# Performance work log

Measured on AMD Instinct MI355X. Metric: run time of the kernel, lower is better.

Reference implementation:

```python
import jax, jax.numpy as jnp
import numpy as np

E = 128       # embedding_size
H = 4         # num_heads
D = E // H    # head_dim = 32
PAD = 16      # window_size; full window width = 2*PAD+1 = 33
B = 4
N = 8192


def setup_inputs() -> dict:
    key = jax.random.key(0)
    ks = jax.random.split(key, 9)
    s = 1.0 / np.sqrt(E)
    return {
        "q": jax.random.normal(ks[0], (B, N, E), dtype=jnp.float32),
        "Wq_w": jax.random.normal(ks[1], (E, E), dtype=jnp.float32) * s,
        "Wq_b": jax.random.normal(ks[2], (E,), dtype=jnp.float32) * s,
        "Wk_w": jax.random.normal(ks[3], (E, E), dtype=jnp.float32) * s,
        "Wk_b": jax.random.normal(ks[4], (E,), dtype=jnp.float32) * s,
        "Wv_w": jax.random.normal(ks[5], (E, E), dtype=jnp.float32) * s,
        "Wv_b": jax.random.normal(ks[6], (E,), dtype=jnp.float32) * s,
        "Wo_w": jax.random.normal(ks[7], (E, E), dtype=jnp.float32) * s,
        "Wo_b": jax.random.normal(ks[8], (E,), dtype=jnp.float32) * s,
    }


def reference(q, Wq_w, Wq_b, Wk_w, Wk_b, Wv_w, Wv_b, Wo_w, Wo_b):
    # Self-attention: k = v = q (forward defaults).
    Q = q @ Wq_w.T + Wq_b
    K = q @ Wk_w.T + Wk_b
    V = q @ Wv_w.T + Wv_b
    b, n, _ = Q.shape
    # (b, H, n, D)
    Q = Q.reshape(b, n, H, D).transpose(0, 2, 1, 3)
    K = K.reshape(b, n, H, D).transpose(0, 2, 1, 3)
    V = V.reshape(b, n, H, D).transpose(0, 2, 1, 3)
    W = 2 * PAD + 1
    # Zero-pad the sequence dim (matches F.pad: padded keys are zero vectors,
    # included in softmax WITHOUT masking — faithful to the original).
    K_pad = jnp.pad(K, ((0, 0), (0, 0), (PAD, PAD), (0, 0)))
    V_pad = jnp.pad(V, ((0, 0), (0, 0), (PAD, PAD), (0, 0)))
    # Window gather indices: row n sees padded positions n .. n+2*PAD
    idx = jnp.arange(n)[:, None] + jnp.arange(W)[None, :]  # (n, W)
    K_win = K_pad[:, :, idx]  # (b, H, n, W, D)
    V_win = V_pad[:, :, idx]  # (b, H, n, W, D)
    scores = jnp.einsum("bhnd,bhnwd->bhnw", Q, K_win) / jnp.sqrt(
        jnp.asarray(D, dtype=Q.dtype)
    )
    probs = jax.nn.softmax(scores, axis=-1)  # dropout is identity in eval
    out = jnp.einsum("bhnw,bhnwd->bhnd", probs, V_win)
    out = out.transpose(0, 2, 1, 3).reshape(b, n, E)
    out = out @ Wo_w.T + Wo_b
    return out, probs
```

## Files before the change

### kernel.cpp

```cpp
#include <hip/hip_runtime.h>

#define BN 4
#define NN 8192
#define EE 128
#define HH 4
#define DD 32
#define WW 33
#define MROWS (BN*NN)
#define QELEMS (MROWS*EE)
#define WELEMS (EE*EE)
#define RT 8

typedef __bf16 bf16x8 __attribute__((ext_vector_type(8)));
typedef float f32x4 __attribute__((ext_vector_type(4)));
typedef unsigned short u16x8 __attribute__((ext_vector_type(8)));

static __device__ __forceinline__ unsigned short f2bf(float x){
    unsigned u = __float_as_uint(x);
    u += 0x7fffu + ((u >> 16) & 1u);
    return (unsigned short)(u >> 16);
}
static __device__ __forceinline__ float bf2f(unsigned short h){
    return __uint_as_float(((unsigned)h) << 16);
}
static __device__ __forceinline__ bf16x8 ld_bf8(const unsigned short* p){
    u16x8 v = *(const u16x8*)p;
    return __builtin_bit_cast(bf16x8, v);
}

__global__ void __launch_bounds__(256) prep_w(const float* __restrict__ wq, const float* __restrict__ wk,
        const float* __restrict__ wv, const float* __restrict__ wo,
        unsigned short* __restrict__ wh, unsigned short* __restrict__ wl){
    int i = blockIdx.x*256 + threadIdx.x;
    int sel = i >> 14;
    const float* src = (sel==0)? wq : (sel==1)? wk : (sel==2)? wv : wo;
    float x = src[i & (WELEMS-1)];
    unsigned short h = f2bf(x);
    wh[i] = h;
    wl[i] = f2bf(x - bf2f(h));
}

__global__ void __launch_bounds__(512,2) gemm_qkv(const float* __restrict__ q,
        const unsigned short* __restrict__ wh, const unsigned short* __restrict__ wl,
        const float* __restrict__ bq, const float* __restrict__ bk, const float* __restrict__ bv_,
        float* __restrict__ Qf, float* __restrict__ Kf, float* __restrict__ Vf)
{
    const int w = threadIdx.x >> 6;
    const int lane = threadIdx.x & 63;
    const int m = lane & 15, g = lane >> 4;
    const int rowB = blockIdx.x * (16*RT);

    bf16x8 bH[3][4], bL[3][4];
    #pragma unroll
    for (int i=0;i<3;i++){
        const unsigned short* WHp = wh + i*WELEMS + (size_t)(w*16 + m)*EE;
        const unsigned short* WLp = wl + i*WELEMS + (size_t)(w*16 + m)*EE;
        #pragma unroll
        for (int kc=0;kc<4;kc++){
            bH[i][kc] = ld_bf8(WHp + kc*32 + g*8);
            bL[i][kc] = ld_bf8(WLp + kc*32 + g*8);
        }
    }
    const float bias[3] = { bq[w*16+m], bk[w*16+m], bv_[w*16+m] };
    float* const outp[3] = { Qf, Kf, Vf };

    float4 fa[2][8];
    {
        const float* qrow = q + (size_t)(rowB + m) * EE;
        #pragma unroll
        for (int kc=0;kc<4;kc++){
            fa[0][kc*2]   = *(const float4*)(qrow + kc*32 + g*8);
            fa[0][kc*2+1] = *(const float4*)(qrow + kc*32 + g*8 + 4);
        }
    }
    #pragma unroll
    for (int rt=0; rt<RT; rt++){
        const int row0 = rowB + rt*16;
        if (rt+1 < RT){
            const float* qrow = q + (size_t)(row0 + 16 + m) * EE;
            #pragma unroll
            for (int kc=0;kc<4;kc++){
                fa[(rt+1)&1][kc*2]   = *(const float4*)(qrow + kc*32 + g*8);
                fa[(rt+1)&1][kc*2+1] = *(const float4*)(qrow + kc*32 + g*8 + 4);
            }
        }
        bf16x8 aH[4], aL[4];
        #pragma unroll
        for (int kc=0;kc<4;kc++){
            float4 v0 = fa[rt&1][kc*2], v1 = fa[rt&1][kc*2+1];
            float vv[8] = {v0.x,v0.y,v0.z,v0.w,v1.x,v1.y,v1.z,v1.w};
            u16x8 hh, ll;
            #pragma unroll
            for (int j=0;j<8;j++){
                unsigned short h = f2bf(vv[j]);
                hh[j] = h;
                ll[j] = f2bf(vv[j] - bf2f(h));
            }
            aH[kc] = __builtin_bit_cast(bf16x8, hh);
            aL[kc] = __builtin_bit_cast(bf16x8, ll);
        }
        #pragma unroll
        for (int i=0;i<3;i++){
            f32x4 acc = {0.f,0.f,0.f,0.f};
            #pragma unroll
            for (int kc=0;kc<4;kc++){
                acc = __builtin_amdgcn_mfma_f32_16x16x32_bf16(aH[kc], bH[i][kc], acc, 0,0,0);
                acc = __builtin_amdgcn_mfma_f32_16x16x32_bf16(aH[kc], bL[i][kc], acc, 0,0,0);
                acc = __builtin_amdgcn_mfma_f32_16x16x32_bf16(aL[kc], bH[i][kc], acc, 0,0,0);
            }
            float* op = outp[i] + (size_t)(row0 + g*4)*EE + w*16 + m;
            #pragma unroll
            for (int r=0;r<4;r++) op[(size_t)r*EE] = acc[r] + bias[i];
        }
    }
}

__global__ void __launch_bounds__(512,2) gemm_o(const unsigned short* __restrict__ ah,
        const unsigned short* __restrict__ al,
        const unsigned short* __restrict__ WHg, const unsigned short* __restrict__ WLg,
        const float* __restrict__ bo, float* __restrict__ out)
{
    const int w = threadIdx.x >> 6;
    const int lane = threadIdx.x & 63;
    const int m = lane & 15, g = lane >> 4;
    const int rowB = blockIdx.x * (16*RT);

    bf16x8 bH[4], bL[4];
    {
        const unsigned short* WHp = WHg + (size_t)(w*16 + m)*EE;
        const unsigned short* WLp = WLg + (size_t)(w*16 + m)*EE;
        #pragma unroll
        for (int kc=0;kc<4;kc++){
            bH[kc] = ld_bf8(WHp + kc*32 + g*8);
            bL[kc] = ld_bf8(WLp + kc*32 + g*8);
        }
    }
    const float biasv = bo[w*16+m];

    bf16x8 fa[2][8];
    {
        const size_t abase = (size_t)(rowB + m) * EE;
        #pragma unroll
        for (int kc=0;kc<4;kc++){
            fa[0][kc]   = ld_bf8(ah + abase + kc*32 + g*8);
            fa[0][4+kc] = ld_bf8(al + abase + kc*32 + g*8);
        }
    }
    #pragma unroll
    for (int rt=0; rt<RT; rt++){
        const int row0 = rowB + rt*16;
        if (rt+1 < RT){
            const size_t abase = (size_t)(row0 + 16 + m) * EE;
            #pragma unroll
            for (int kc=0;kc<4;kc++){
                fa[(rt+1)&1][kc]   = ld_bf8(ah + abase + kc*32 + g*8);
                fa[(rt+1)&1][4+kc] = ld_bf8(al + abase + kc*32 + g*8);
            }
        }
        f32x4 acc = {0.f,0.f,0.f,0.f};
        #pragma unroll
        for (int kc=0;kc<4;kc++){
            acc = __builtin_amdgcn_mfma_f32_16x16x32_bf16(fa[rt&1][kc],   bH[kc], acc, 0,0,0);
            acc = __builtin_amdgcn_mfma_f32_16x16x32_bf16(fa[rt&1][kc],   bL[kc], acc, 0,0,0);
            acc = __builtin_amdgcn_mfma_f32_16x16x32_bf16(fa[rt&1][4+kc], bH[kc], acc, 0,0,0);
        }
        float* op = out + (size_t)(row0 + g*4)*EE + w*16 + m;
        #pragma unroll
        for (int r=0;r<4;r++) op[(size_t)r*EE] = acc[r] + biasv;
    }
}

__global__ void __launch_bounds__(256) attn_kernel(const float* __restrict__ Qf,
        const float* __restrict__ Kf, const float* __restrict__ Vf,
        float* __restrict__ probs, unsigned short* __restrict__ ah, unsigned short* __restrict__ al)
{
    __shared__ float Kl[96*33];
    __shared__ float Vl[96*33];
    __shared__ float Pl[64*WW];
    const int t = threadIdx.x;
    const int bh = blockIdx.y;
    const int b = bh >> 2, h = bh & 3;
    const int n0 = blockIdx.x * 64;
    const size_t rowbase = (size_t)b * NN;

    #pragma unroll
    for (int i=0;i<3;i++){
        int idx = t + i*256;
        int row = idx >> 3, q4 = idx & 7;
        int grow = n0 - 16 + row;
        float4 kv = make_float4(0.f,0.f,0.f,0.f);
        float4 vv = make_float4(0.f,0.f,0.f,0.f);
        if (grow >= 0 && grow < NN){
            size_t goff = (rowbase + grow)*EE + h*DD + q4*4;
            kv = *(const float4*)(Kf + goff);
            vv = *(const float4*)(Vf + goff);
        }
        int lo = row*33 + q4*4;
        *(float4*)(Kl + lo) = kv;
        *(float4*)(Vl + lo) = vv;
    }
    __syncthreads();

    const int p = t >> 2, e = t & 3;
    const int n = n0 + p;

    float qr[8];
    {
        const float4* qp = (const float4*)(Qf + (rowbase + n)*EE + h*DD + e*8);
        float4 v0 = qp[0], v1 = qp[1];
        qr[0]=v0.x; qr[1]=v0.y; qr[2]=v0.z; qr[3]=v0.w;
        qr[4]=v1.x; qr[5]=v1.y; qr[6]=v1.z; qr[7]=v1.w;
    }

    float sc[WW];
    #pragma unroll
    for (int w=0; w<WW; w++){
        const float* kr = &Kl[(p+w)*33 + e*8];
        float s = 0.f;
        #pragma unroll
        for (int k=0;k<8;k++) s = fmaf(qr[k], kr[k], s);
        sc[w] = s;
    }
    #pragma unroll
    for (int w=0; w<WW; w++){
        float s = sc[w];
        s += __shfl_xor(s, 1);
        s += __shfl_xor(s, 2);
        sc[w] = s * 0.17677669529663687f;
    }

    float mx = sc[0];
    #pragma unroll
    for (int w=1;w<WW;w++) mx = fmaxf(mx, sc[w]);
    float sum = 0.f;
    #pragma unroll
    for (int w=0;w<WW;w++){ sc[w] = __expf(sc[w]-mx); sum += sc[w]; }
    float inv = 1.f / sum;
    #pragma unroll
    for (int w=0;w<WW;w++) sc[w] *= inv;

    {
        float* pl = Pl + p*WW;
        if (e==0){
            #pragma unroll
            for (int w=0;w<9;w++) pl[w] = sc[w];
        } else if (e==1){
            #pragma unroll
            for (int w=9;w<17;w++) pl[w] = sc[w];
        } else if (e==2){
            #pragma unroll
            for (int w=17;w<25;w++) pl[w] = sc[w];
        } else {
            #pragma unroll
            for (int w=25;w<WW;w++) pl[w] = sc[w];
        }
    }

    float acc[8];
    #pragma unroll
    for (int k=0;k<8;k++) acc[k]=0.f;
    #pragma unroll
    for (int w=0;w<WW;w++){
        const float* vr = &Vl[(p+w)*33 + e*8];
        float pw = sc[w];
        #pragma unroll
        for (int k=0;k<8;k++) acc[k] = fmaf(pw, vr[k], acc[k]);
    }

    unsigned short hi[8], lo2[8];
    #pragma unroll
    for (int k=0;k<8;k++){ hi[k]=f2bf(acc[k]); lo2[k]=f2bf(acc[k]-bf2f(hi[k])); }
    size_t aoff = (rowbase + n)*EE + h*DD + e*8;
    *(ushort4*)(ah + aoff)     = make_ushort4(hi[0],hi[1],hi[2],hi[3]);
    *(ushort4*)(ah + aoff + 4) = make_ushort4(hi[4],hi[5],hi[6],hi[7]);
    *(ushort4*)(al + aoff)     = make_ushort4(lo2[0],lo2[1],lo2[2],lo2[3]);
    *(ushort4*)(al + aoff + 4) = make_ushort4(lo2[4],lo2[5],lo2[6],lo2[7]);

    __syncthreads();
    float* pbase = probs + ((size_t)bh*NN + n0)*WW;
    #pragma unroll
    for (int i=0;i<9;i++){
        int idx = t + i*256;
        if (idx < 64*WW) pbase[idx] = Pl[idx];
    }
}

extern "C" void kernel_launch(void* const* d_in, const int* in_sizes, int n_in,
                              void* d_out, int out_size, void* d_ws, size_t ws_size,
                              hipStream_t stream) {
    const float* q  = (const float*)d_in[0];
    const float* Wq = (const float*)d_in[1];  const float* bq = (const float*)d_in[2];
    const float* Wk = (const float*)d_in[3];  const float* bk = (const float*)d_in[4];
    const float* Wv = (const float*)d_in[5];  const float* bv = (const float*)d_in[6];
    const float* Wo = (const float*)d_in[7];  const float* bo = (const float*)d_in[8];

    float* out   = (float*)d_out;
    float* probs = out + QELEMS;

    unsigned short* a_hi = (unsigned short*)d_ws;
    unsigned short* a_lo = a_hi + QELEMS;
    unsigned short* w_hi = a_lo + QELEMS;
    unsigned short* w_lo = w_hi + 4*WELEMS;
    float* Qf = (float*)(w_lo + 4*WELEMS);
    float* Kf = Qf + QELEMS;
    float* Vf = Kf + QELEMS;

    prep_w<<<4*WELEMS/256, 256, 0, stream>>>(Wq, Wk, Wv, Wo, w_hi, w_lo);
    gemm_qkv<<<dim3(MROWS/(16*RT), 1), 512, 0, stream>>>(q, w_hi, w_lo,
                                                         bq, bk, bv, Qf, Kf, Vf);
    attn_kernel<<<dim3(NN/64, BN*HH), 256, 0, stream>>>(Qf, Kf, Vf, probs, a_hi, a_lo);
    gemm_o<<<dim3(MROWS/(16*RT), 1), 512, 0, stream>>>(a_hi, a_lo,
                                                       w_hi + 3*WELEMS, w_lo + 3*WELEMS, bo, out);
}
```

Measured before the change: 161.7 us.

## Fuse QKV projection, windowed attention and output projection into one kernel

```diff
diff --git a/kernel.cpp b/kernel.cpp
--- a/kernel.cpp
+++ b/kernel.cpp
@@ -9,7 +9,6 @@
 #define MROWS (BN*NN)
 #define QELEMS (MROWS*EE)
 #define WELEMS (EE*EE)
-#define RT 8
 
 typedef __bf16 bf16x8 __attribute__((ext_vector_type(8)));
 typedef float f32x4 __attribute__((ext_vector_type(4)));
@@ -40,67 +39,80 @@
     wl[i] = f2bf(x - bf2f(h));
 }
 
-__global__ void __launch_bounds__(512,2) gemm_qkv(const float* __restrict__ q,
+__global__ void __launch_bounds__(512,2) fused_kernel(
+        const float* __restrict__ q,
         const unsigned short* __restrict__ wh, const unsigned short* __restrict__ wl,
         const float* __restrict__ bq, const float* __restrict__ bk, const float* __restrict__ bv_,
-        float* __restrict__ Qf, float* __restrict__ Kf, float* __restrict__ Vf)
+        const float* __restrict__ bo,
+        float* __restrict__ out, float* __restrict__ probs)
 {
-    const int w = threadIdx.x >> 6;
-    const int lane = threadIdx.x & 63;
+    __shared__ float Kl[HH*96*33];
+    __shared__ float Vl[HH*96*33];
+    __shared__ float Ql[HH*64*33];
+
+    const int t = threadIdx.x;
+    const int wv = t >> 6;
+    const int lane = t & 63;
     const int m = lane & 15, g = lane >> 4;
-    const int rowB = blockIdx.x * (16*RT);
+    const int b = blockIdx.y;
+    const int n0 = blockIdx.x * 64;
+    const size_t qrow0 = (size_t)b * NN;
 
     bf16x8 bH[3][4], bL[3][4];
     #pragma unroll
     for (int i=0;i<3;i++){
-        const unsigned short* WHp = wh + i*WELEMS + (size_t)(w*16 + m)*EE;
-        const unsigned short* WLp = wl + i*WELEMS + (size_t)(w*16 + m)*EE;
-        #pragma unroll
-        for (int kc=0;kc<4;kc++){
-            bH[i][kc] = ld_bf8(WHp + kc*32 + g*8);
-            bL[i][kc] = ld_bf8(WLp + kc*32 + g*8);
-        }
-    }
-    const float bias[3] = { bq[w*16+m], bk[w*16+m], bv_[w*16+m] };
-    float* const outp[3] = { Qf, Kf, Vf };
+        const unsigned short* WH = wh + i*WELEMS + (size_t)(wv*16+m)*EE;
+        const unsigned short* WL = wl + i*WELEMS + (size_t)(wv*16+m)*EE;
+        #pragma unroll
+        for (int kc=0;kc<4;kc++){
+            bH[i][kc] = ld_bf8(WH + kc*32 + g*8);
+            bL[i][kc] = ld_bf8(WL + kc*32 + g*8);
+        }
+    }
+    const float bias3[3] = { bq[wv*16+m], bk[wv*16+m], bv_[wv*16+m] };
+    const int head = wv >> 1, dimb = (wv & 1) * 16;
 
     float4 fa[2][8];
     {
-        const float* qrow = q + (size_t)(rowB + m) * EE;
-        #pragma unroll
-        for (int kc=0;kc<4;kc++){
-            fa[0][kc*2]   = *(const float4*)(qrow + kc*32 + g*8);
-            fa[0][kc*2+1] = *(const float4*)(qrow + kc*32 + g*8 + 4);
-        }
-    }
-    #pragma unroll
-    for (int rt=0; rt<RT; rt++){
-        const int row0 = rowB + rt*16;
-        if (rt+1 < RT){
-            const float* qrow = q + (size_t)(row0 + 16 + m) * EE;
+        int grow = n0 - 16 + m;
+        bool ok = (grow >= 0) && (grow < NN);
+        const float* qp = q + (qrow0 + (ok ? grow : 0))*EE;
+        #pragma unroll
+        for (int kc=0;kc<4;kc++){
+            fa[0][kc*2]   = ok ? *(const float4*)(qp + kc*32 + g*8)     : make_float4(0.f,0.f,0.f,0.f);
+            fa[0][kc*2+1] = ok ? *(const float4*)(qp + kc*32 + g*8 + 4) : make_float4(0.f,0.f,0.f,0.f);
+        }
+    }
+    #pragma unroll
+    for (int tile=0; tile<6; tile++){
+        if (tile < 5){
+            int grow = n0 - 16 + (tile+1)*16 + m;
+            bool ok = (grow >= 0) && (grow < NN);
+            const float* qp = q + (qrow0 + (ok ? grow : 0))*EE;
             #pragma unroll
             for (int kc=0;kc<4;kc++){
-                fa[(rt+1)&1][kc*2]   = *(const float4*)(qrow + kc*32 + g*8);
-                fa[(rt+1)&1][kc*2+1] = *(const float4*)(qrow + kc*32 + g*8 + 4);
+                fa[(tile+1)&1][kc*2]   = ok ? *(const float4*)(qp + kc*32 + g*8)     : make_float4(0.f,0.f,0.f,0.f);
+                fa[(tile+1)&1][kc*2+1] = ok ? *(const float4*)(qp + kc*32 + g*8 + 4) : make_float4(0.f,0.f,0.f,0.f);
             }
         }
         bf16x8 aH[4], aL[4];
         #pragma unroll
         for (int kc=0;kc<4;kc++){
-            float4 v0 = fa[rt&1][kc*2], v1 = fa[rt&1][kc*2+1];
-            float vv[8] = {v0.x,v0.y,v0.z,v0.w,v1.x,v1.y,v1.z,v1.w};
+            float4 v0 = fa[tile&1][kc*2], v1 = fa[tile&1][kc*2+1];
+            float vvv[8] = {v0.x,v0.y,v0.z,v0.w,v1.x,v1.y,v1.z,v1.w};
             u16x8 hh, ll;
             #pragma unroll
             for (int j=0;j<8;j++){
-                unsigned short h = f2bf(vv[j]);
-                hh[j] = h;
-                ll[j] = f2bf(vv[j] - bf2f(h));
+                unsigned short hB = f2bf(vvv[j]);
+                hh[j] = hB;
+                ll[j] = f2bf(vvv[j] - bf2f(hB));
             }
             aH[kc] = __builtin_bit_cast(bf16x8, hh);
             aL[kc] = __builtin_bit_cast(bf16x8, ll);
         }
         #pragma unroll
         for (int i=0;i<3;i++){
+            if (i==0 && (tile==0 || tile==5)) continue;
             f32x4 acc = {0.f,0.f,0.f,0.f};
             #pragma unroll
             for (int kc=0;kc<4;kc++){
@@ -108,180 +120,137 @@
                 acc = __builtin_amdgcn_mfma_f32_16x16x32_bf16(aH[kc], bL[i][kc], acc, 0,0,0);
                 acc = __builtin_amdgcn_mfma_f32_16x16x32_bf16(aL[kc], bH[i][kc], acc, 0,0,0);
             }
-            float* op = outp[i] + (size_t)(row0 + g*4)*EE + w*16 + m;
-            #pragma unroll
-            for (int r=0;r<4;r++) op[(size_t)r*EE] = acc[r] + bias[i];
-        }
-    }
-}
-
-__global__ void __launch_bounds__(512,2) gemm_o(const unsigned short* __restrict__ ah,
-        const unsigned short* __restrict__ al,
-        const unsigned short* __restrict__ WHg, const unsigned short* __restrict__ WLg,
-        const float* __restrict__ bo, float* __restrict__ out)
-{
-    const int w = threadIdx.x >> 6;
-    const int lane = threadIdx.x & 63;
-    const int m = lane & 15, g = lane >> 4;
-    const int rowB = blockIdx.x * (16*RT);
-
-    bf16x8 bH[4], bL[4];
-    {
-        const unsigned short* WHp = WHg + (size_t)(w*16 + m)*EE;
-        const unsigned short* WLp = WLg + (size_t)(w*16 + m)*EE;
-        #pragma unroll
-        for (int kc=0;kc<4;kc++){
-            bH[kc] = ld_bf8(WHp + kc*32 + g*8);
-            bL[kc] = ld_bf8(WLp + kc*32 + g*8);
-        }
-    }
-    const float biasv = bo[w*16+m];
-
-    bf16x8 fa[2][8];
-    {
-        const size_t abase = (size_t)(rowB + m) * EE;
-        #pragma unroll
-        for (int kc=0;kc<4;kc++){
-            fa[0][kc]   = ld_bf8(ah + abase + kc*32 + g*8);
-            fa[0][4+kc] = ld_bf8(al + abase + kc*32 + g*8);
-        }
-    }
-    #pragma unroll
-    for (int rt=0; rt<RT; rt++){
-        const int row0 = rowB + rt*16;
-        if (rt+1 < RT){
-            const size_t abase = (size_t)(row0 + 16 + m) * EE;
-            #pragma unroll
-            for (int kc=0;kc<4;kc++){
-                fa[(rt+1)&1][kc]   = ld_bf8(ah + abase + kc*32 + g*8);
-                fa[(rt+1)&1][4+kc] = ld_bf8(al + abase + kc*32 + g*8);
-            }
-        }
-        f32x4 acc = {0.f,0.f,0.f,0.f};
-        #pragma unroll
-        for (int kc=0;kc<4;kc++){
-            acc = __builtin_amdgcn_mfma_f32_16x16x32_bf16(fa[rt&1][kc],   bH[kc], acc, 0,0,0);
-            acc = __builtin_amdgcn_mfma_f32_16x16x32_bf16(fa[rt&1][kc],   bL[kc], acc, 0,0,0);
-            acc = __builtin_amdgcn_mfma_f32_16x16x32_bf16(fa[rt&1][4+kc], bH[kc], acc, 0,0,0);
-        }
-        float* op = out + (size_t)(row0 + g*4)*EE + w*16 + m;
-        #pragma unroll
-        for (int r=0;r<4;r++) op[(size_t)r*EE] = acc[r] + biasv;
-    }
-}
-
-__global__ void __launch_bounds__(256) attn_kernel(const float* __restrict__ Qf,
-        const float* __restrict__ Kf, const float* __restrict__ Vf,
-        float* __restrict__ probs, unsigned short* __restrict__ ah, unsigned short* __restrict__ al)
-{
-    __shared__ float Kl[96*33];
-    __shared__ float Vl[96*33];
-    __shared__ float Pl[64*WW];
-    const int t = threadIdx.x;
-    const int bh = blockIdx.y;
-    const int b = bh >> 2, h = bh & 3;
-    const int n0 = blockIdx.x * 64;
-    const size_t rowbase = (size_t)b * NN;
-
-    #pragma unroll
-    for (int i=0;i<3;i++){
-        int idx = t + i*256;
-        int row = idx >> 3, q4 = idx & 7;
-        int grow = n0 - 16 + row;
-        float4 kv = make_float4(0.f,0.f,0.f,0.f);
-        float4 vv = make_float4(0.f,0.f,0.f,0.f);
-        if (grow >= 0 && grow < NN){
-            size_t goff = (rowbase + grow)*EE + h*DD + q4*4;
-            kv = *(const float4*)(Kf + goff);
-            vv = *(const float4*)(Vf + goff);
-        }
-        int lo = row*33 + q4*4;
-        *(float4*)(Kl + lo) = kv;
-        *(float4*)(Vl + lo) = vv;
+            #pragma unroll
+            for (int r=0;r<4;r++){
+                int hrow = tile*16 + g*4 + r;
+                int grow = n0 - 16 + hrow;
+                bool inr = (grow >= 0) && (grow < NN);
+                float val = acc[r] + (inr ? bias3[i] : 0.f);
+                if (i==0)      Ql[(head*64 + hrow-16)*33 + dimb + m] = val;
+                else if (i==1) Kl[(head*96 + hrow   )*33 + dimb + m] = val;
+                else           Vl[(head*96 + hrow   )*33 + dimb + m] = val;
+            }
+        }
     }
     __syncthreads();
 
-    const int p = t >> 2, e = t & 3;
-    const int n = n0 + p;
-
-    float qr[8];
-    {
-        const float4* qp = (const float4*)(Qf + (rowbase + n)*EE + h*DD + e*8);
-        float4 v0 = qp[0], v1 = qp[1];
-        qr[0]=v0.x; qr[1]=v0.y; qr[2]=v0.z; qr[3]=v0.w;
-        qr[4]=v1.x; qr[5]=v1.y; qr[6]=v1.z; qr[7]=v1.w;
-    }
-
+    const int pr = t >> 1, e = t & 1;
+    const int p = pr & 63, h = pr >> 6;
+    float qr[16];
+    {
+        const float* qlp = &Ql[(h*64 + p)*33 + e*16];
+        #pragma unroll
+        for (int k=0;k<16;k++) qr[k] = qlp[k];
+    }
     float sc[WW];
     #pragma unroll
-    for (int w=0; w<WW; w++){
-        const float* kr = &Kl[(p+w)*33 + e*8];
+    for (int ww=0; ww<WW; ww++){
+        const float* kr = &Kl[(h*96 + p + ww)*33 + e*16];
         float s = 0.f;
         #pragma unroll
-        for (int k=0;k<8;k++) s = fmaf(qr[k], kr[k], s);
-        sc[w] = s;
-    }
-    #pragma unroll
-    for (int w=0; w<WW; w++){
-        float s = sc[w];
-        s += __shfl_xor(s, 1);
-        s += __shfl_xor(s, 2);
-        sc[w] = s * 0.17677669529663687f;
-    }
+        for (int k=0;k<16;k++) s = fmaf(qr[k], kr[k], s);
+        sc[ww] = s;
+    }
+    #pragma unroll
+    for (int ww=0; ww<WW; ww++)
+        sc[ww] = (sc[ww] + __shfl_xor(sc[ww], 1)) * 0.17677669529663687f;
+
+    __syncthreads();
 
     float mx = sc[0];
     #pragma unroll
-    for (int w=1;w<WW;w++) mx = fmaxf(mx, sc[w]);
+    for (int ww=1;ww<WW;ww++) mx = fmaxf(mx, sc[ww]);
     float sum = 0.f;
     #pragma unroll
-    for (int w=0;w<WW;w++){ sc[w] = __expf(sc[w]-mx); sum += sc[w]; }
+    for (int ww=0;ww<WW;ww++){ sc[ww] = __expf(sc[ww]-mx); sum += sc[ww]; }
     float inv = 1.f / sum;
     #pragma unroll
-    for (int w=0;w<WW;w++) sc[w] *= inv;
-
-    {
-        float* pl = Pl + p*WW;
+    for (int ww=0;ww<WW;ww++) sc[ww] *= inv;
+
+    float* Pst = Ql;
+    {
+        float* pl = Pst + (h*64 + p)*33;
         if (e==0){
             #pragma unroll
-            for (int w=0;w<9;w++) pl[w] = sc[w];
-        } else if (e==1){
-            #pragma unroll
-            for (int w=9;w<17;w++) pl[w] = sc[w];
-        } else if (e==2){
-            #pragma unroll
-            for (int w=17;w<25;w++) pl[w] = sc[w];
+            for (int ww=0;ww<17;ww++) pl[ww] = sc[ww];
         } else {
             #pragma unroll
-            for (int w=25;w<WW;w++) pl[w] = sc[w];
-        }
-    }
-
-    float acc[8];
-    #pragma unroll
-    for (int k=0;k<8;k++) acc[k]=0.f;
-    #pragma unroll
-    for (int w=0;w<WW;w++){
-        const float* vr = &Vl[(p+w)*33 + e*8];
-        float pw = sc[w];
-        #pragma unroll
-        for (int k=0;k<8;k++) acc[k] = fmaf(pw, vr[k], acc[k]);
-    }
-
-    unsigned short hi[8], lo2[8];
-    #pragma unroll
-    for (int k=0;k<8;k++){ hi[k]=f2bf(acc[k]); lo2[k]=f2bf(acc[k]-bf2f(hi[k])); }
-    size_t aoff = (rowbase + n)*EE + h*DD + e*8;
-    *(ushort4*)(ah + aoff)     = make_ushort4(hi[0],hi[1],hi[2],hi[3]);
-    *(ushort4*)(ah + aoff + 4) = make_ushort4(hi[4],hi[5],hi[6],hi[7]);
-    *(ushort4*)(al + aoff)     = make_ushort4(lo2[0],lo2[1],lo2[2],lo2[3]);
-    *(ushort4*)(al + aoff + 4) = make_ushort4(lo2[4],lo2[5],lo2[6],lo2[7]);
-
+            for (int ww=17;ww<WW;ww++) pl[ww] = sc[ww];
+        }
+    }
+
+    float pv[16];
+    #pragma unroll
+    for (int k=0;k<16;k++) pv[k]=0.f;
+    #pragma unroll
+    for (int ww=0;ww<WW;ww++){
+        const float* vr = &Vl[(h*96 + p + ww)*33 + e*16];
+        float pw = sc[ww];
+        #pragma unroll
+        for (int k=0;k<16;k++) pv[k] = fmaf(pw, vr[k], pv[k]);
+    }
+
+    unsigned int* Au = (unsigned int*)Kl;
+    {
+        unsigned int* ap = Au + p*132 + h*32 + e*16;
+        #pragma unroll
+        for (int k=0;k<16;k++){
+            unsigned short hB = f2bf(pv[k]);
+            unsigned short lB = f2bf(pv[k] - bf2f(hB));
+            ap[k] = ((unsigned)hB << 16) | (unsigned)lB;
+        }
+    }
     __syncthreads();
-    float* pbase = probs + ((size_t)bh*NN + n0)*WW;
-    #pragma unroll
-    for (int i=0;i<9;i++){
-        int idx = t + i*256;
-        if (idx < 64*WW) pbase[idx] = Pl[idx];
+
+    bf16x8 cH[4], cL[4];
+    {
+        const unsigned short* WH = wh + 3*WELEMS + (size_t)(wv*16+m)*EE;
+        const unsigned short* WL = wl + 3*WELEMS + (size_t)(wv*16+m)*EE;
+        #pragma unroll
+        for (int kc=0;kc<4;kc++){
+            cH[kc] = ld_bf8(WH + kc*32 + g*8);
+            cL[kc] = ld_bf8(WL + kc*32 + g*8);
+        }
+    }
+    const float bov = bo[wv*16+m];
+
+    #pragma unroll
+    for (int i2=0;i2<17;i2++){
+        int idx = t + i2*512;
+        if (idx < HH*64*WW){
+            int hh2 = idx / (64*WW);
+            int rr  = idx - hh2*(64*WW);
+            probs[((size_t)(b*HH + hh2)*NN + n0)*WW + rr] = Pst[idx];
+        }
+    }
+
+    #pragma unroll
+    for (int rt=0; rt<4; rt++){
+        bf16x8 aH2[4], aL2[4];
+        const unsigned int* ap = Au + (rt*16 + m)*132;
+        #pragma unroll
+        for (int kc=0;kc<4;kc++){
+            const unsigned int* app = ap + kc*32 + g*8;
+            u16x8 hh, ll;
+            #pragma unroll
+            for (int j=0;j<8;j++){
+                unsigned int u = app[j];
+                hh[j] = (unsigned short)(u >> 16);
+                ll[j] = (unsigned short)(u & 0xffffu);
+            }
+            aH2[kc] = __builtin_bit_cast(bf16x8, hh);
+            aL2[kc] = __builtin_bit_cast(bf16x8, ll);
+        }
+        f32x4 acc2 = {0.f,0.f,0.f,0.f};
+        #pragma unroll
+        for (int kc=0;kc<4;kc++){
+            acc2 = __builtin_amdgcn_mfma_f32_16x16x32_bf16(aH2[kc], cH[kc], acc2, 0,0,0);
+            acc2 = __builtin_amdgcn_mfma_f32_16x16x32_bf16(aH2[kc], cL[kc], acc2, 0,0,0);
+            acc2 = __builtin_amdgcn_mfma_f32_16x16x32_bf16(aL2[kc], cH[kc], acc2, 0,0,0);
+        }
+        float* op = out + (qrow0 + n0 + rt*16 + g*4)*EE + wv*16 + m;
+        #pragma unroll
+        for (int r=0;r<4;r++) op[(size_t)r*EE] = acc2[r] + bov;
     }
 }
 
@@ -297,18 +266,10 @@
     float* out   = (float*)d_out;
     float* probs = out + QELEMS;
 
-    unsigned short* a_hi = (unsigned short*)d_ws;
-    unsigned short* a_lo = a_hi + QELEMS;
-    unsigned short* w_hi = a_lo + QELEMS;
+    unsigned short* w_hi = (unsigned short*)d_ws;
     unsigned short* w_lo = w_hi + 4*WELEMS;
-    float* Qf = (float*)(w_lo + 4*WELEMS);
-    float* Kf = Qf + QELEMS;
-    float* Vf = Kf + QELEMS;
 
     prep_w<<<4*WELEMS/256, 256, 0, stream>>>(Wq, Wk, Wv, Wo, w_hi, w_lo);
-    gemm_qkv<<<dim3(MROWS/(16*RT), 1), 512, 0, stream>>>(q, w_hi, w_lo,
-                                                         bq, bk, bv, Qf, Kf, Vf);
-    attn_kernel<<<dim3(NN/64, BN*HH), 256, 0, stream>>>(Qf, Kf, Vf, probs, a_hi, a_lo);
-    gemm_o<<<dim3(MROWS/(16*RT), 1), 512, 0, stream>>>(a_hi, a_lo,
-                                                       w_hi + 3*WELEMS, w_lo + 3*WELEMS, bo, out);
-}
+    fused_kernel<<<dim3(NN/64, BN), 512, 0, stream>>>(q, w_hi, w_lo,
+                                                      bq, bk, bv, bo, out, probs);
+}
```

After: 149.7 us. 7.5% less time.
